# Performance work log

Measured on AMD Instinct MI355X. Metric: run time of the kernel, lower is better.

Reference implementation:

```python
import jax, jax.numpy as jnp
import numpy as np

B, NUM_RX, NUM_CHIRPS, SAMPLES = 16, 4, 64, 256
D_BINS, R_BINS = 64, 256


def _conv3d(x, w, b, pad):
    y = jax.lax.conv_general_dilated(x, w, (1, 1, 1), pad,
                                     dimension_numbers=('NCDHW', 'OIDHW', 'NCDHW'))
    return y + b[None, :, None, None, None]


def _conv2d(x, w, b, pad):
    y = jax.lax.conv_general_dilated(x, w, (1, 1), pad,
                                     dimension_numbers=('NCHW', 'OIHW', 'NCHW'))
    return y + b[None, :, None, None]


def _bn2(x, s, t):
    return x * s[None, :, None, None] + t[None, :, None, None]


def _bn3(x, s, t):
    return x * s[None, :, None, None, None] + t[None, :, None, None, None]


def _upsample_bilinear_ac(x, oh, ow):
    # torch Upsample(mode='bilinear', align_corners=True)
    _, _, h, w = x.shape
    ph = jnp.linspace(0.0, h - 1.0, oh)
    pw = jnp.linspace(0.0, w - 1.0, ow)
    h0 = jnp.clip(jnp.floor(ph).astype(jnp.int32), 0, h - 1)
    h1 = jnp.clip(h0 + 1, 0, h - 1)
    fh = ph - h0
    w0 = jnp.clip(jnp.floor(pw).astype(jnp.int32), 0, w - 1)
    w1 = jnp.clip(w0 + 1, 0, w - 1)
    fw = pw - w0
    x = x[:, :, h0, :] * (1.0 - fh)[None, None, :, None] + x[:, :, h1, :] * fh[None, None, :, None]
    x = x[:, :, :, w0] * (1.0 - fw) + x[:, :, :, w1] * fw
    return x


def setup_inputs() -> dict:
    ks = iter(jax.random.split(jax.random.key(0), 80))

    def nrm(shape, s=0.05):
        return s * jax.random.normal(next(ks), shape, dtype=jnp.float32)

    inp = {'x': jax.random.normal(next(ks), (B, NUM_RX, NUM_CHIRPS, SAMPLES, 2), dtype=jnp.float32)}

    def conv(name, shape):
        inp[name + '_w'] = nrm(shape)
        inp[name + '_b'] = nrm((shape[0],))

    def bn(name, n):  # BatchNorm in inference form folded to scale/shift
        inp[name + '_s'] = 1.0 + nrm((n,), 0.1)
        inp[name + '_t'] = nrm((n,), 0.1)

    conv('tc1', (16, 2, 1, 1, 3)); bn('tc1', 16)
    conv('tc2', (32, 16, 1, 1, 3)); bn('tc2', 32)
    conv('rx', (32, 32, NUM_RX, 1, 1)); bn('rx', 32)
    conv('cc1', (64, 32 * NUM_CHIRPS, 3, 3)); bn('cc1', 64)
    conv('cc2', (64, 64, 3, 3)); bn('cc2', 64)
    conv('rd1', (128, 64, 3, 3)); bn('rd1', 128)
    conv('rd2', (128, 128, 3, 3)); bn('rd2', 128)
    conv('up1', (64, 128, 3, 3)); bn('up1', 64)
    conv('up2', (32, 64, 3, 3)); bn('up2', 32)
    conv('up3', (1, 32, 1, 1))
    inp['wr'] = jax.random.normal(next(ks), (SAMPLES, R_BINS, 2), dtype=jnp.float32)
    inp['wd'] = jax.random.normal(next(ks), (NUM_CHIRPS, D_BINS, 2), dtype=jnp.float32)
    return inp


def reference(x, tc1_w, tc1_b, tc1_s, tc1_t, tc2_w, tc2_b, tc2_s, tc2_t,
              rx_w, rx_b, rx_s, rx_t, cc1_w, cc1_b, cc1_s, cc1_t,
              cc2_w, cc2_b, cc2_s, cc2_t, rd1_w, rd1_b, rd1_s, rd1_t,
              rd2_w, rd2_b, rd2_s, rd2_t, up1_w, up1_b, up1_s, up1_t,
              up2_w, up2_b, up2_s, up2_t, up3_w, up3_b, wr, wd):
    r = jax.nn.relu
    p3 = [(0, 0), (0, 0), (1, 1)]
    p2 = [(1, 1), (1, 1)]
    h = jnp.transpose(x, (0, 4, 1, 2, 3))                      # [B,2,RX,C,S]
    h = r(_bn3(_conv3d(h, tc1_w, tc1_b, p3), tc1_s, tc1_t))
    h = r(_bn3(_conv3d(h, tc2_w, tc2_b, p3), tc2_s, tc2_t))
    h = r(_bn3(_conv3d(h, rx_w, rx_b, [(0, 0)] * 3), rx_s, rx_t))[:, :, 0]  # [B,32,C,S]
    h = h.reshape(h.shape[0], -1, SAMPLES)[:, :, None, :]      # [B,32*C,1,S]
    h = r(_bn2(_conv2d(h, cc1_w, cc1_b, p2), cc1_s, cc1_t))
    h = r(_bn2(_conv2d(h, cc2_w, cc2_b, p2), cc2_s, cc2_t))
    h = r(_bn2(_conv2d(h, rd1_w, rd1_b, p2), rd1_s, rd1_t))
    h = r(_bn2(_conv2d(h, rd2_w, rd2_b, p2), rd2_s, rd2_t))
    h = _upsample_bilinear_ac(h, D_BINS, R_BINS)               # [B,128,D,R]
    h = r(_bn2(_conv2d(h, up1_w, up1_b, p2), up1_s, up1_t))
    h = r(_bn2(_conv2d(h, up2_w, up2_b, p2), up2_s, up2_t))
    h = jax.nn.sigmoid(_conv2d(h, up3_w, up3_b, [(0, 0), (0, 0)]))  # [B,1,D,R]
    # learnable_fft (input is real: x_imag = 0), loops -> two batched matmuls
    xr = h[:, 0]                                               # [B,D,R]
    rr = jnp.einsum('bcs,sr->bcr', xr, wr[:, :, 0])            # range DFT, real
    ri = jnp.einsum('bcs,sr->bcr', xr, wr[:, :, 1])            # range DFT, imag
    rdr = jnp.einsum('bcr,cd->bdr', rr, wd[:, :, 0]) - jnp.einsum('bcr,cd->bdr', ri, wd[:, :, 1])
    rdi = jnp.einsum('bcr,cd->bdr', rr, wd[:, :, 1]) + jnp.einsum('bcr,cd->bdr', ri, wd[:, :, 0])
    mag = jnp.sqrt(rdr * rdr + rdi * rdi) / (NUM_CHIRPS * SAMPLES)
    out = jnp.clip(h + 0.1 * mag[:, None], 0.0, 1.0)
    return jnp.transpose(out, (0, 2, 3, 1))                    # [B,D,R,1]
```

## Files before the change

kernel.cpp:

```cpp
#include <hip/hip_runtime.h>
#include <math.h>

#define OFF_A      0u
#define OFF_P      8388608u
#define OFF_WCC1   10485760u
#define OFF_BCC1   11010048u
#define OFF_WCC2   11010112u
#define OFF_BCC2   11026496u
#define OFF_WRD1   11026560u
#define OFF_BRD1   11059328u
#define OFF_WRD2   11059456u
#define OFF_BRD2   11124992u
#define OFF_WUP1   11125120u
#define OFF_BUP1   11223424u
#define OFF_WUP2   11223488u
#define OFF_BUP2   11346368u
#define OFF_WRX    11346400u
#define OFF_W1F    11350496u
#define OFF_B1F    11350592u
#define OFF_W2F    11350608u
#define OFF_B2F    11352144u
#define OFF_BRXF   11352176u
#define OFF_R      0u
#define OFF_H      524288u

__device__ __forceinline__ void fma4(float4& a, const float4& x, float w) {
  a.x = fmaf(x.x, w, a.x); a.y = fmaf(x.y, w, a.y);
  a.z = fmaf(x.z, w, a.z); a.w = fmaf(x.w, w, a.w);
}

__global__ __launch_bounds__(256) void k_repack_front(
    const float* __restrict__ tc1_w, const float* __restrict__ tc1_b, const float* __restrict__ tc1_s, const float* __restrict__ tc1_t,
    const float* __restrict__ tc2_w, const float* __restrict__ tc2_b, const float* __restrict__ tc2_s, const float* __restrict__ tc2_t,
    const float* __restrict__ rx_w, const float* __restrict__ rx_b, const float* __restrict__ rx_s, const float* __restrict__ rx_t,
    float* __restrict__ ws)
{
  const int tid = blockIdx.x * blockDim.x + threadIdx.x;
  const int nth = gridDim.x * blockDim.x;
  for (int i = tid; i < 96; i += nth) ws[OFF_W1F + i] = tc1_w[i] * tc1_s[i/6];
  for (int i = tid; i < 16; i += nth) ws[OFF_B1F + i] = tc1_b[i]*tc1_s[i] + tc1_t[i];
  for (int i = tid; i < 1536; i += nth) {
    int oc = i & 31, r = i >> 5, k = r % 3, ic = r / 3;
    ws[OFF_W2F + i] = tc2_w[oc*48 + ic*3 + k] * tc2_s[oc];
  }
  for (int i = tid; i < 32; i += nth) ws[OFF_B2F + i] = tc2_b[i]*tc2_s[i] + tc2_t[i];
  for (int i = tid; i < 4096; i += nth) {
    int oc = i & 31, ic = (i >> 5) & 31, rxi = i >> 10;
    ws[OFF_WRX + i] = rx_w[(oc*32 + ic)*4 + rxi] * rx_s[oc];
  }
  for (int i = tid; i < 32; i += nth) ws[OFF_BRXF + i] = rx_b[i]*rx_s[i] + rx_t[i];
}

__global__ __launch_bounds__(256, 4) void k_front(
    const float* __restrict__ x, const float* __restrict__ ws_c, float* __restrict__ ws,
    const float* __restrict__ cc1_w, const float* __restrict__ cc1_b, const float* __restrict__ cc1_s, const float* __restrict__ cc1_t,
    const float* __restrict__ cc2_w, const float* __restrict__ cc2_b, const float* __restrict__ cc2_s, const float* __restrict__ cc2_t,
    const float* __restrict__ rd1_w, const float* __restrict__ rd1_b, const float* __restrict__ rd1_s, const float* __restrict__ rd1_t,
    const float* __restrict__ rd2_w, const float* __restrict__ rd2_b, const float* __restrict__ rd2_s, const float* __restrict__ rd2_t,
    const float* __restrict__ up1_w, const float* __restrict__ up1_b, const float* __restrict__ up1_s, const float* __restrict__ up1_t,
    const float* __restrict__ up2_w, const float* __restrict__ up2_b, const float* __restrict__ up2_s, const float* __restrict__ up2_t,
    float* __restrict__ A)
{
  __shared__ float t1s[16][258];
  const int tid = threadIdx.x;

  if (blockIdx.x < 64) {
    const int t = blockIdx.x * 256 + tid;
    const int nth = 64 * 256;
    for (int i = t; i < 2048*64*4; i += nth) {
      int k = i & 3, oc = (i >> 2) & 63, c2 = i >> 8;
      ws[OFF_WCC1 + i] = (k < 3) ? cc1_w[((oc*2048 + c2)*3 + 1)*3 + k] * cc1_s[oc] : 0.f;
    }
    for (int i = t; i < 64; i += nth) ws[OFF_BCC1 + i] = cc1_b[i]*cc1_s[i] + cc1_t[i];
    for (int i = t; i < 64*64; i += nth) {
      int oc = i & 63, ic = i >> 6;
      float4 v;
      v.x = cc2_w[(oc*64 + ic)*9 + 3] * cc2_s[oc];
      v.y = cc2_w[(oc*64 + ic)*9 + 4] * cc2_s[oc];
      v.z = cc2_w[(oc*64 + ic)*9 + 5] * cc2_s[oc];
      v.w = 0.f;
      ((float4*)(ws + OFF_WCC2))[i] = v;
    }
    for (int i = t; i < 64; i += nth) ws[OFF_BCC2 + i] = cc2_b[i]*cc2_s[i] + cc2_t[i];
    for (int i = t; i < 64*128; i += nth) {
      int oc = i & 127, ic = i >> 7;
      float4 v;
      v.x = rd1_w[(oc*64 + ic)*9 + 3] * rd1_s[oc];
      v.y = rd1_w[(oc*64 + ic)*9 + 4] * rd1_s[oc];
      v.z = rd1_w[(oc*64 + ic)*9 + 5] * rd1_s[oc];
      v.w = 0.f;
      ((float4*)(ws + OFF_WRD1))[i] = v;
    }
    for (int i = t; i < 128; i += nth) ws[OFF_BRD1 + i] = rd1_b[i]*rd1_s[i] + rd1_t[i];
    for (int i = t; i < 128*128; i += nth) {
      int oc = i & 127, ic = i >> 7;
      float4 v;
      v.x = rd2_w[(oc*128 + ic)*9 + 3] * rd2_s[oc];
      v.y = rd2_w[(oc*128 + ic)*9 + 4] * rd2_s[oc];
      v.z = rd2_w[(oc*128 + ic)*9 + 5] * rd2_s[oc];
      v.w = 0.f;
      ((float4*)(ws + OFF_WRD2))[i] = v;
    }
    for (int i = t; i < 128; i += nth) ws[OFF_BRD2 + i] = rd2_b[i]*rd2_s[i] + rd2_t[i];
    for (int i = t; i < 3*128*64; i += nth) {
      int oc = i & 63, ic = (i >> 6) & 127, v = i >> 13;
      const int m = (v == 0) ? 6 : (v == 1) ? 7 : 3;
      float4 o = make_float4(0.f, 0.f, 0.f, 0.f);
      for (int kh = 0; kh < 3; ++kh)
        if ((m >> kh) & 1) {
          o.x += up1_w[((oc*128 + ic)*3 + kh)*3 + 0];
          o.y += up1_w[((oc*128 + ic)*3 + kh)*3 + 1];
          o.z += up1_w[((oc*128 + ic)*3 + kh)*3 + 2];
        }
      o.x *= up1_s[oc]; o.y *= up1_s[oc]; o.z *= up1_s[oc];
      ((float4*)(ws + OFF_WUP1))[i] = o;
    }
    for (int i = t; i < 64; i += nth) ws[OFF_BUP1 + i] = up1_b[i]*up1_s[i] + up1_t[i];
    for (int i = t; i < 5*3*64*32; i += nth) {
      int oc = i & 31, ic = (i >> 5) & 63, tt = i >> 11;
      int src = tt % 3, v = tt / 3;
      const int MASKS[15] = {2,4,0,  1,6,0,  0,7,0,  0,3,4,  0,1,2};
      const int m = MASKS[v*3 + src];
      float4 o = make_float4(0.f, 0.f, 0.f, 0.f);
      for (int kh = 0; kh < 3; ++kh)
        if ((m >> kh) & 1) {
          o.x += up2_w[((oc*64 + ic)*3 + kh)*3 + 0];
          o.y += up2_w[((oc*64 + ic)*3 + kh)*3 + 1];
          o.z += up2_w[((oc*64 + ic)*3 + kh)*3 + 2];
        }
      o.x *= up2_s[oc]; o.y *= up2_s[oc]; o.z *= up2_s[oc];
      ((float4*)(ws + OFF_WUP2))[i] = o;
    }
    for (int i = t; i < 32; i += nth) ws[OFF_BUP2 + i] = up2_b[i]*up2_s[i] + up2_t[i];
    return;
  }

  const int bb = blockIdx.x - 64;
  const int b = bb >> 6, chirp = bb & 63;
  const int s = tid;

  if (tid < 32) { int o = tid & 15; int c = (tid >> 4) ? 257 : 0; t1s[o][c] = 0.f; }

  const float* w1f  = ws_c + OFF_W1F;
  const float* b1f  = ws_c + OFF_B1F;
  const float* w2f  = ws_c + OFF_W2F;
  const float* b2f  = ws_c + OFF_B2F;
  const float* wrxf = ws_c + OFF_WRX;
  const float* brxf = ws_c + OFF_BRXF;

  float acc[32];
  #pragma unroll
  for (int j = 0; j < 32; ++j) acc[j] = 0.f;

  #pragma unroll 1
  for (int rxi = 0; rxi < 4; ++rxi) {
    {
      const float2* xb2 = (const float2*)(x + ((size_t)(((b*4 + rxi)*64 + chirp)*256) << 1));
      float2 xm = xb2[s];
      float2 xl = xb2[(s == 0) ? 0 : (s - 1)];
      float2 xr = xb2[(s == 255) ? 255 : (s + 1)];
      if (s == 0)   { xl.x = 0.f; xl.y = 0.f; }
      if (s == 255) { xr.x = 0.f; xr.y = 0.f; }
      #pragma unroll 4
      for (int o = 0; o < 16; ++o) {
        const float* w = w1f + o*6;
        float v = b1f[o];
        v = fmaf(xl.x, w[0], v);
        v = fmaf(xm.x, w[1], v);
        v = fmaf(xr.x, w[2], v);
        v = fmaf(xl.y, w[3], v);
        v = fmaf(xm.y, w[4], v);
        v = fmaf(xr.y, w[5], v);
        t1s[o][s+1] = fmaxf(v, 0.f);
      }
    }
    __syncthreads();

    float t2[32];
    #pragma unroll
    for (int j = 0; j < 32; ++j) t2[j] = b2f[j];
    #pragma unroll 2
    for (int ic = 0; ic < 16; ++ic) {
      float tl = t1s[ic][s];
      float tm = t1s[ic][s+1];
      float tr = t1s[ic][s+2];
      const float* w = w2f + ic*96;
      #pragma unroll
      for (int oc = 0; oc < 32; ++oc)
        t2[oc] = fmaf(tl, w[oc], fmaf(tm, w[32+oc], fmaf(tr, w[64+oc], t2[oc])));
    }
    #pragma unroll
    for (int j = 0; j < 32; ++j) t2[j] = fmaxf(t2[j], 0.f);

    const float* wr0 = wrxf + rxi*1024;
    #pragma unroll 4
    for (int ic = 0; ic < 32; ++ic) {
      float tv = t2[ic];
      const float* w = wr0 + ic*32;
      #pragma unroll
      for (int oc = 0; oc < 32; ++oc)
        acc[oc] = fmaf(tv, w[oc], acc[oc]);
    }
    __syncthreads();
  }

  #pragma unroll 4
  for (int oc = 0; oc < 32; ++oc) {
    float v = fmaxf(acc[oc] + brxf[oc], 0.f);
    A[(size_t)((b*2048 + oc*64 + chirp)*256) + s] = v;
  }
}

__global__ __launch_bounds__(256) void k_cc1(
    const float* __restrict__ A, const float* __restrict__ wp, float* __restrict__ P)
{
  __shared__ __align__(16) float As[256][36];
  const int tid = threadIdx.x;
  const int ks = blockIdx.x & 7;
  const int stile = (blockIdx.x >> 3) & 7;
  const int b = blockIdx.x >> 6;
  const int s0 = stile * 32;
  const int oc = tid & 63;
  const int sg = tid >> 6;
  const int cbase = ks * 256;
  const float4* w4 = (const float4*)wp;

  for (int i = tid; i < 256*36; i += 256) {
    int c = i / 36, si = i - c*36;
    int sA = s0 - 1 + si;
    float v = 0.f;
    if (si < 34 && sA >= 0 && sA < 256)
      v = A[(size_t)(b*2048 + cbase + c)*256 + sA];
    As[c][si] = v;
  }
  __syncthreads();

  const int sb = sg * 8;
  float4 acc0 = make_float4(0.f,0.f,0.f,0.f);
  float4 acc1 = make_float4(0.f,0.f,0.f,0.f);
  #pragma unroll 4
  for (int c = 0; c < 256; ++c) {
    float4 w = w4[(size_t)(cbase + c)*64 + oc];
    float4 a0 = *(const float4*)&As[c][sb];
    float4 a1 = *(const float4*)&As[c][sb + 4];
    float2 a2 = *(const float2*)&As[c][sb + 8];
    acc0.x = fmaf(a0.x,w.x, fmaf(a0.y,w.y, fmaf(a0.z,w.z, acc0.x)));
    acc0.y = fmaf(a0.y,w.x, fmaf(a0.z,w.y, fmaf(a0.w,w.z, acc0.y)));
    acc0.z = fmaf(a0.z,w.x, fmaf(a0.w,w.y, fmaf(a1.x,w.z, acc0.z)));
    acc0.w = fmaf(a0.w,w.x, fmaf(a1.x,w.y, fmaf(a1.y,w.z, acc0.w)));
    acc1.x = fmaf(a1.x,w.x, fmaf(a1.y,w.y, fmaf(a1.z,w.z, acc1.x)));
    acc1.y = fmaf(a1.y,w.x, fmaf(a1.z,w.y, fmaf(a1.w,w.z, acc1.y)));
    acc1.z = fmaf(a1.z,w.x, fmaf(a1.w,w.y, fmaf(a2.x,w.z, acc1.z)));
    acc1.w = fmaf(a1.w,w.x, fmaf(a2.x,w.y, fmaf(a2.y,w.z, acc1.w)));
  }
  float* Pk = P + ((size_t)(ks*16 + b)*256)*64;
  int s = s0 + sb;
  Pk[(size_t)(s+0)*64 + oc] = acc0.x;
  Pk[(size_t)(s+1)*64 + oc] = acc0.y;
  Pk[(size_t)(s+2)*64 + oc] = acc0.z;
  Pk[(size_t)(s+3)*64 + oc] = acc0.w;
  Pk[(size_t)(s+4)*64 + oc] = acc1.x;
  Pk[(size_t)(s+5)*64 + oc] = acc1.y;
  Pk[(size_t)(s+6)*64 + oc] = acc1.z;
  Pk[(size_t)(s+7)*64 + oc] = acc1.w;
}

__global__ __launch_bounds__(256) void k_mid(
    const float* __restrict__ P, const float* __restrict__ bcc1,
    const float* __restrict__ wcc2, const float* __restrict__ bcc2,
    const float* __restrict__ wrd1, const float* __restrict__ brd1,
    const float* __restrict__ wrd2, const float* __restrict__ brd2,
    float* __restrict__ R)
{
  __shared__ __align__(16) float c1s[64][20];
  __shared__ __align__(16) float c2s[64][20];
  __shared__ __align__(16) float r1s[128][12];
  const int tid = threadIdx.x;
  const int b = blockIdx.x >> 5;
  const int s0 = (blockIdx.x & 31) * 8;
  const float4* wc2 = (const float4*)wcc2;
  const float4* wr1 = (const float4*)wrd1;
  const float4* wr2 = (const float4*)wrd2;

  for (int i = tid; i < 64*14; i += 256) {
    int ic = i & 63, si = i >> 6;
    int sA = s0 - 3 + si;
    float v = 0.f;
    if (sA >= 0 && sA < 256) {
      float a = bcc1[ic];
      #pragma unroll
      for (int ksp = 0; ksp < 8; ++ksp)
        a += P[((size_t)(ksp*16 + b)*256 + sA)*64 + ic];
      v = fmaxf(a, 0.f);
    }
    c1s[ic][si] = v;
  }
  __syncthreads();

  {
    const int g = tid >> 6, oc = tid & 63;
    if (g < 3) {
      float bb = bcc2[oc];
      float4 acc = make_float4(bb, bb, bb, bb);
      #pragma unroll 4
      for (int ic = 0; ic < 64; ++ic) {
        float4 w = wc2[ic*64 + oc];
        float4 ca = *(const float4*)&c1s[ic][g*4];
        float2 cb = *(const float2*)&c1s[ic][g*4 + 4];
        acc.x = fmaf(ca.x,w.x, fmaf(ca.y,w.y, fmaf(ca.z,w.z, acc.x)));
        acc.y = fmaf(ca.y,w.x, fmaf(ca.z,w.y, fmaf(ca.w,w.z, acc.y)));
        acc.z = fmaf(ca.z,w.x, fmaf(ca.w,w.y, fmaf(cb.x,w.z, acc.z)));
        acc.w = fmaf(ca.w,w.x, fmaf(cb.x,w.y, fmaf(cb.y,w.z, acc.w)));
      }
      c2s[oc][g*4+0] = fmaxf(acc.x, 0.f);
      c2s[oc][g*4+1] = fmaxf(acc.y, 0.f);
      c2s[oc][g*4+2] = fmaxf(acc.z, 0.f);
      c2s[oc][g*4+3] = fmaxf(acc.w, 0.f);
    } else {
      int oc2 = tid - 192;
      c2s[oc2][12] = 0.f;
      c2s[oc2][13] = 0.f;
    }
  }
  __syncthreads();

  for (int it = tid; it < 384; it += 256) {
    const int oc = it & 127, g = it >> 7;
    float bb = brd1[oc];
    float4 acc = make_float4(bb, bb, bb, bb);
    #pragma unroll 4
    for (int ic = 0; ic < 64; ++ic) {
      float4 w = wr1[ic*128 + oc];
      float4 ca = *(const float4*)&c2s[ic][g*4];
      float2 cb = *(const float2*)&c2s[ic][g*4 + 4];
      acc.x = fmaf(ca.x,w.x, fmaf(ca.y,w.y, fmaf(ca.z,w.z, acc.x)));
      acc.y = fmaf(ca.y,w.x, fmaf(ca.z,w.y, fmaf(ca.w,w.z, acc.y)));
      acc.z = fmaf(ca.z,w.x, fmaf(ca.w,w.y, fmaf(cb.x,w.z, acc.z)));
      acc.w = fmaf(ca.w,w.x, fmaf(cb.x,w.y, fmaf(cb.y,w.z, acc.w)));
    }
    if (g*4 + 0 < 12) r1s[oc][g*4+0] = fmaxf(acc.x, 0.f);
    if (g*4 + 1 < 12) r1s[oc][g*4+1] = fmaxf(acc.y, 0.f);
    if (g*4 + 2 < 12) r1s[oc][g*4+2] = fmaxf(acc.z, 0.f);
    if (g*4 + 3 < 12) r1s[oc][g*4+3] = fmaxf(acc.w, 0.f);
  }
  __syncthreads();

  {
    const int g = tid >> 7, oc = tid & 127;
    float bb = brd2[oc];
    float4 acc = make_float4(bb, bb, bb, bb);
    #pragma unroll 4
    for (int ic = 0; ic < 128; ++ic) {
      float4 w = wr2[ic*128 + oc];
      float4 ca = *(const float4*)&r1s[ic][g*4];
      float2 cb = *(const float2*)&r1s[ic][g*4 + 4];
      acc.x = fmaf(ca.x,w.x, fmaf(ca.y,w.y, fmaf(ca.z,w.z, acc.x)));
      acc.y = fmaf(ca.y,w.x, fmaf(ca.z,w.y, fmaf(ca.w,w.z, acc.y)));
      acc.z = fmaf(ca.z,w.x, fmaf(ca.w,w.y, fmaf(cb.x,w.z, acc.z)));
      acc.w = fmaf(ca.w,w.x, fmaf(cb.x,w.y, fmaf(cb.y,w.z, acc.w)));
    }
    int s = s0 + g*4;
    R[((size_t)b*256 + s+0)*128 + oc] = fmaxf(acc.x, 0.f);
    R[((size_t)b*256 + s+1)*128 + oc] = fmaxf(acc.y, 0.f);
    R[((size_t)b*256 + s+2)*128 + oc] = fmaxf(acc.z, 0.f);
    R[((size_t)b*256 + s+3)*128 + oc] = fmaxf(acc.w, 0.f);
  }
}

__global__ __launch_bounds__(192) void k_up(
    const float* __restrict__ R,
    const float* __restrict__ wup1, const float* __restrict__ bup1,
    const float* __restrict__ wup2, const float* __restrict__ bup2,
    const float* __restrict__ up3_w, const float* __restrict__ up3_b,
    float* __restrict__ H)
{
  __shared__ __align__(16) float Rs[128][12];
  __shared__ __align__(16) float u1s[3][64][12];
  __shared__ float u2s[5][32][9];
  const int tid = threadIdx.x;
  const int b = blockIdx.x >> 5;
  const int s0 = (blockIdx.x & 31) * 8;

  for (int i = tid; i < 128*12; i += 192) {
    int ic = i & 127, si = i >> 7;
    int sA = s0 - 2 + si;
    Rs[ic][si] = (sA >= 0 && sA < 256) ? R[((size_t)b*256 + sA)*128 + ic] : 0.f;
  }
  __syncthreads();

  {
    const int vi = tid >> 6, oc = tid & 63;
    const float4* w4 = (const float4*)wup1;
    float a[10];
    float bb = bup1[oc];
    #pragma unroll
    for (int p = 0; p < 10; ++p) a[p] = bb;
    #pragma unroll 4
    for (int ic = 0; ic < 128; ++ic) {
      float4 w = w4[(vi*128 + ic)*64 + oc];
      float4 ra = *(const float4*)&Rs[ic][0];
      float4 rb = *(const float4*)&Rs[ic][4];
      float4 rc = *(const float4*)&Rs[ic][8];
      float r[12] = {ra.x,ra.y,ra.z,ra.w, rb.x,rb.y,rb.z,rb.w, rc.x,rc.y,rc.z,rc.w};
      #pragma unroll
      for (int p = 0; p < 10; ++p)
        a[p] = fmaf(r[p],w.x, fmaf(r[p+1],w.y, fmaf(r[p+2],w.z, a[p])));
    }
    #pragma unroll
    for (int p = 0; p < 10; ++p) u1s[vi][oc][p] = fmaxf(a[p], 0.f);
    u1s[vi][oc][10] = 0.f; u1s[vi][oc][11] = 0.f;
  }
  __syncthreads();

  if (tid < 160) {
    const int v = tid >> 5, oc = tid & 31;
    const float4* w4 = (const float4*)wup2;
    float a[8];
    float bb = bup2[oc];
    #pragma unroll
    for (int p = 0; p < 8; ++p) a[p] = bb;
    for (int src = 0; src < 3; ++src) {
      #pragma unroll 4
      for (int ic = 0; ic < 64; ++ic) {
        float4 w = w4[((v*3 + src)*64 + ic)*32 + oc];
        float4 ua = *(const float4*)&u1s[src][ic][0];
        float4 ub = *(const float4*)&u1s[src][ic][4];
        float2 uc = *(const float2*)&u1s[src][ic][8];
        float r[10] = {ua.x,ua.y,ua.z,ua.w, ub.x,ub.y,ub.z,ub.w, uc.x,uc.y};
        #pragma unroll
        for (int p = 0; p < 8; ++p)
          a[p] = fmaf(r[p],w.x, fmaf(r[p+1],w.y, fmaf(r[p+2],w.z, a[p])));
      }
    }
    #pragma unroll
    for (int p = 0; p < 8; ++p) u2s[v][oc][p] = fmaxf(a[p], 0.f);
  }
  __syncthreads();

  if (tid < 40) {
    int v = tid >> 3, j = tid & 7;
    float a = up3_b[0];
    for (int ic = 0; ic < 32; ++ic)
      a = fmaf(u2s[v][ic][j], up3_w[ic], a);
    H[(size_t)(b*5 + v)*256 + s0 + j] = 1.f / (1.f + expf(-a));
  }
}

__global__ __launch_bounds__(256) void k_spec(
    const float* __restrict__ H, const float* __restrict__ wr, const float* __restrict__ wd,
    float* __restrict__ out)
{
  __shared__ float hs[5][256];
  __shared__ float S0[64], S1[64];
  __shared__ float wds[4][64][2];
  __shared__ float ps[16][16][10];
  __shared__ float rred[16][10];
  const int tid = threadIdx.x;
  const int b = blockIdx.x >> 4;
  const int rt = blockIdx.x & 15;
  const int r0 = rt * 16;

  for (int i = tid; i < 1280; i += 256) hs[i >> 8][i & 255] = H[(size_t)b*1280 + i];
  if (tid < 64) {
    const float2* wd2 = (const float2*)wd;
    float a0 = 0.f, a1 = 0.f;
    for (int c = 2; c <= 61; ++c) {
      float2 v = wd2[c*64 + tid];
      a0 += v.x; a1 += v.y;
    }
    S0[tid] = a0; S1[tid] = a1;
  }
  for (int i = tid; i < 512; i += 256) {
    int row = i >> 7, rem = i & 127, d = rem >> 1, comp = rem & 1;
    int c = (row < 2) ? row : (60 + row);
    wds[row][d][comp] = wd[(c*64 + d)*2 + comp];
  }
  __syncthreads();

  {
    const int rl = tid & 15;
    const int sq = tid >> 4;
    const int r = r0 + rl;
    float rr[5] = {0,0,0,0,0}, ri[5] = {0,0,0,0,0};
    const float2* wr2p = (const float2*)wr;
    for (int s = sq*16; s < sq*16 + 16; ++s) {
      float2 w = wr2p[s*256 + r];
      #pragma unroll
      for (int k = 0; k < 5; ++k) {
        float hv = hs[k][s];
        rr[k] = fmaf(hv, w.x, rr[k]);
        ri[k] = fmaf(hv, w.y, ri[k]);
      }
    }
    #pragma unroll
    for (int k = 0; k < 5; ++k) {
      ps[sq][rl][k]     = rr[k];
      ps[sq][rl][5 + k] = ri[k];
    }
  }
  __syncthreads();

  if (tid < 160) {
    const int rl = tid & 15, k = tid >> 4;
    float a = 0.f;
    #pragma unroll
    for (int sq = 0; sq < 16; ++sq) a += ps[sq][rl][k];
    rred[rl][k] = a;
  }
  __syncthreads();

  {
    const int rl = tid & 15, dg = tid >> 4;
    const int r = r0 + rl;
    float Rr[5], Ri[5];
    #pragma unroll
    for (int k = 0; k < 5; ++k) { Rr[k] = rred[rl][k]; Ri[k] = rred[rl][5 + k]; }
    for (int dd = 0; dd < 4; ++dd) {
      int d = dg*4 + dd;
      float w0r = wds[0][d][0], w0i = wds[0][d][1];
      float w1r = wds[1][d][0], w1i = wds[1][d][1];
      float w2r = wds[2][d][0], w2i = wds[2][d][1];
      float w3r = wds[3][d][0], w3i = wds[3][d][1];
      float s0v = S0[d], s1v = S1[d];
      float rdr = Rr[0]*w0r + Rr[1]*w1r + Rr[2]*s0v + Rr[3]*w2r + Rr[4]*w3r
                - Ri[0]*w0i - Ri[1]*w1i - Ri[2]*s1v - Ri[3]*w2i - Ri[4]*w3i;
      float rdi = Rr[0]*w0i + Rr[1]*w1i + Rr[2]*s1v + Rr[3]*w2i + Rr[4]*w3i
                + Ri[0]*w0r + Ri[1]*w1r + Ri[2]*s0v + Ri[3]*w2r + Ri[4]*w3r;
      float mag = sqrtf(rdr*rdr + rdi*rdi) * (1.0f / 16384.0f);
      int v = (d == 0) ? 0 : (d == 1) ? 1 : (d <= 61) ? 2 : ((d == 62) ? 3 : 4);
      float o = hs[v][r] + 0.1f * mag;
      out[(size_t)b*16384 + d*256 + r] = fminf(fmaxf(o, 0.f), 1.f);
    }
  }
}

extern "C" void kernel_launch(void* const* d_in, const int* in_sizes, int n_in,
                              void* d_out, int out_size, void* d_ws, size_t ws_size,
                              hipStream_t stream)
{
  const float* x     = (const float*)d_in[0];
  const float* tc1_w = (const float*)d_in[1];  const float* tc1_b = (const float*)d_in[2];
  const float* tc1_s = (const float*)d_in[3];  const float* tc1_t = (const float*)d_in[4];
  const float* tc2_w = (const float*)d_in[5];  const float* tc2_b = (const float*)d_in[6];
  const float* tc2_s = (const float*)d_in[7];  const float* tc2_t = (const float*)d_in[8];
  const float* rx_w  = (const float*)d_in[9];  const float* rx_b  = (const float*)d_in[10];
  const float* rx_s  = (const float*)d_in[11]; const float* rx_t  = (const float*)d_in[12];
  const float* cc1_w = (const float*)d_in[13]; const float* cc1_b = (const float*)d_in[14];
  const float* cc1_s = (const float*)d_in[15]; const float* cc1_t = (const float*)d_in[16];
  const float* cc2_w = (const float*)d_in[17]; const float* cc2_b = (const float*)d_in[18];
  const float* cc2_s = (const float*)d_in[19]; const float* cc2_t = (const float*)d_in[20];
  const float* rd1_w = (const float*)d_in[21]; const float* rd1_b = (const float*)d_in[22];
  const float* rd1_s = (const float*)d_in[23]; const float* rd1_t = (const float*)d_in[24];
  const float* rd2_w = (const float*)d_in[25]; const float* rd2_b = (const float*)d_in[26];
  const float* rd2_s = (const float*)d_in[27]; const float* rd2_t = (const float*)d_in[28];
  const float* up1_w = (const float*)d_in[29]; const float* up1_b = (const float*)d_in[30];
  const float* up1_s = (const float*)d_in[31]; const float* up1_t = (const float*)d_in[32];
  const float* up2_w = (const float*)d_in[33]; const float* up2_b = (const float*)d_in[34];
  const float* up2_s = (const float*)d_in[35]; const float* up2_t = (const float*)d_in[36];
  const float* up3_w = (const float*)d_in[37]; const float* up3_b = (const float*)d_in[38];
  const float* wr    = (const float*)d_in[39];
  const float* wd    = (const float*)d_in[40];
  float* ws  = (float*)d_ws;
  float* out = (float*)d_out;

  k_repack_front<<<8, 256, 0, stream>>>(tc1_w, tc1_b, tc1_s, tc1_t,
                                        tc2_w, tc2_b, tc2_s, tc2_t,
                                        rx_w, rx_b, rx_s, rx_t, ws);
  k_front<<<1088, 256, 0, stream>>>(x, ws, ws,
                                    cc1_w, cc1_b, cc1_s, cc1_t,
                                    cc2_w, cc2_b, cc2_s, cc2_t,
                                    rd1_w, rd1_b, rd1_s, rd1_t,
                                    rd2_w, rd2_b, rd2_s, rd2_t,
                                    up1_w, up1_b, up1_s, up1_t,
                                    up2_w, up2_b, up2_s, up2_t,
                                    ws + OFF_A);
  k_cc1<<<1024, 256, 0, stream>>>(ws + OFF_A, ws + OFF_WCC1, ws + OFF_P);
  k_mid<<<512, 256, 0, stream>>>(ws + OFF_P, ws + OFF_BCC1,
                                 ws + OFF_WCC2, ws + OFF_BCC2,
                                 ws + OFF_WRD1, ws + OFF_BRD1,
                                 ws + OFF_WRD2, ws + OFF_BRD2, ws + OFF_R);
  k_up<<<512, 192, 0, stream>>>(ws + OFF_R, ws + OFF_WUP1, ws + OFF_BUP1,
                                ws + OFF_WUP2, ws + OFF_BUP2, up3_w, up3_b, ws + OFF_H);
  k_spec<<<256, 256, 0, stream>>>(ws + OFF_H, wr, wd, out);
}
```

Baseline: 339.1 us.

## Fuse mid and upsample kernels with halo recompute; double-buffer front t1s per RX pair

New measurement: 357.6 us. 5.5% more time.

```diff
diff --git a/kernel.cpp b/kernel.cpp
--- a/kernel.cpp
+++ b/kernel.cpp
@@ -21,8 +21,7 @@
 #define OFF_W2F    11350608u
 #define OFF_B2F    11352144u
 #define OFF_BRXF   11352176u
-#define OFF_R      0u
-#define OFF_H      524288u
+#define OFF_H      0u
 
 __device__ __forceinline__ void fma4(float4& a, const float4& x, float w) {
   a.x = fmaf(x.x, w, a.x); a.y = fmaf(x.y, w, a.y);
@@ -61,7 +60,7 @@
     const float* __restrict__ up2_w, const float* __restrict__ up2_b, const float* __restrict__ up2_s, const float* __restrict__ up2_t,
     float* __restrict__ A)
 {
-  __shared__ float t1s[16][258];
+  __shared__ float t1s[2][16][258];
   const int tid = threadIdx.x;
 
   if (blockIdx.x < 64) {
@@ -139,7 +138,11 @@
   const int b = bb >> 6, chirp = bb & 63;
   const int s = tid;
 
-  if (tid < 32) { int o = tid & 15; int c = (tid >> 4) ? 257 : 0; t1s[o][c] = 0.f; }
+  if (tid < 64) {
+    int o = tid & 15, rr = (tid >> 4) & 1;
+    int c = (tid >> 5) ? 257 : 0;
+    t1s[rr][o][c] = 0.f;
+  }
 
   const float* w1f  = ws_c + OFF_W1F;
   const float* b1f  = ws_c + OFF_B1F;
@@ -153,8 +156,10 @@
   for (int j = 0; j < 32; ++j) acc[j] = 0.f;
 
   #pragma unroll 1
-  for (int rxi = 0; rxi < 4; ++rxi) {
-    {
+  for (int r2 = 0; r2 < 2; ++r2) {
+    #pragma unroll
+    for (int rr = 0; rr < 2; ++rr) {
+      const int rxi = r2*2 + rr;
       const float2* xb2 = (const float2*)(x + ((size_t)(((b*4 + rxi)*64 + chirp)*256) << 1));
       float2 xm = xb2[s];
       float2 xl = xb2[(s == 0) ? 0 : (s - 1)];
@@ -171,35 +176,39 @@
         v = fmaf(xl.y, w[3], v);
         v = fmaf(xm.y, w[4], v);
         v = fmaf(xr.y, w[5], v);
-        t1s[o][s+1] = fmaxf(v, 0.f);
+        t1s[rr][o][s+1] = fmaxf(v, 0.f);
       }
     }
     __syncthreads();
 
-    float t2[32];
-    #pragma unroll
-    for (int j = 0; j < 32; ++j) t2[j] = b2f[j];
-    #pragma unroll 2
-    for (int ic = 0; ic < 16; ++ic) {
-      float tl = t1s[ic][s];
-      float tm = t1s[ic][s+1];
-      float tr = t1s[ic][s+2];
-      const float* w = w2f + ic*96;
-      #pragma unroll
-      for (int oc = 0; oc < 32; ++oc)
-        t2[oc] = fmaf(tl, w[oc], fmaf(tm, w[32+oc], fmaf(tr, w[64+oc], t2[oc])));
-    }
-    #pragma unroll
-    for (int j = 0; j < 32; ++j) t2[j] = fmaxf(t2[j], 0.f);
-
-    const float* wr0 = wrxf + rxi*1024;
-    #pragma unroll 4
-    for (int ic = 0; ic < 32; ++ic) {
-      float tv = t2[ic];
-      const float* w = wr0 + ic*32;
-      #pragma unroll
-      for (int oc = 0; oc < 32; ++oc)
-        acc[oc] = fmaf(tv, w[oc], acc[oc]);
+    #pragma unroll 1
+    for (int rr = 0; rr < 2; ++rr) {
+      const int rxi = r2*2 + rr;
+      float t2[32];
+      #pragma unroll
+      for (int j = 0; j < 32; ++j) t2[j] = b2f[j];
+      #pragma unroll 2
+      for (int ic = 0; ic < 16; ++ic) {
+        float tl = t1s[rr][ic][s];
+        float tm = t1s[rr][ic][s+1];
+        float tr = t1s[rr][ic][s+2];
+        const float* w = w2f + ic*96;
+        #pragma unroll
+        for (int oc = 0; oc < 32; ++oc)
+          t2[oc] = fmaf(tl, w[oc], fmaf(tm, w[32+oc], fmaf(tr, w[64+oc], t2[oc])));
+      }
+      #pragma unroll
+      for (int j = 0; j < 32; ++j) t2[j] = fmaxf(t2[j], 0.f);
+
+      const float* wr0 = wrxf + rxi*1024;
+      #pragma unroll 4
+      for (int ic = 0; ic < 32; ++ic) {
+        float tv = t2[ic];
+        const float* w = wr0 + ic*32;
+        #pragma unroll
+        for (int oc = 0; oc < 32; ++oc)
+          acc[oc] = fmaf(tv, w[oc], acc[oc]);
+      }
     }
     __syncthreads();
   }
@@ -265,26 +274,37 @@
   Pk[(size_t)(s+7)*64 + oc] = acc1.w;
 }
 
-__global__ __launch_bounds__(256) void k_mid(
+__global__ __launch_bounds__(256) void k_midup(
     const float* __restrict__ P, const float* __restrict__ bcc1,
     const float* __restrict__ wcc2, const float* __restrict__ bcc2,
     const float* __restrict__ wrd1, const float* __restrict__ brd1,
     const float* __restrict__ wrd2, const float* __restrict__ brd2,
-    float* __restrict__ R)
+    const float* __restrict__ wup1, const float* __restrict__ bup1,
+    const float* __restrict__ wup2, const float* __restrict__ bup2,
+    const float* __restrict__ up3_w, const float* __restrict__ up3_b,
+    float* __restrict__ H)
 {
-  __shared__ __align__(16) float c1s[64][20];
-  __shared__ __align__(16) float c2s[64][20];
-  __shared__ __align__(16) float r1s[128][12];
+  __shared__ __align__(16) float bufA[2560];
+  __shared__ __align__(16) float bufB[2560];
+  __shared__ float u2s[5][32][9];
+  float* c1s = bufA;
+  float* c2s = bufA + 1280;
+  float* r1s = bufB;
+  float* Rls = bufA;
+  float* u1s = bufB;
+
   const int tid = threadIdx.x;
   const int b = blockIdx.x >> 5;
   const int s0 = (blockIdx.x & 31) * 8;
   const float4* wc2 = (const float4*)wcc2;
   const float4* wr1 = (const float4*)wrd1;
   const float4* wr2 = (const float4*)wrd2;
-
-  for (int i = tid; i < 64*14; i += 256) {
+  const float4* wu1 = (const float4*)wup1;
+  const float4* wu2 = (const float4*)wup2;
+
+  for (int i = tid; i < 18*64; i += 256) {
     int ic = i & 63, si = i >> 6;
-    int sA = s0 - 3 + si;
+    int sA = s0 - 5 + si;
     float v = 0.f;
     if (sA >= 0 && sA < 256) {
       float a = bcc1[ic];
@@ -293,128 +313,127 @@
         a += P[((size_t)(ksp*16 + b)*256 + sA)*64 + ic];
       v = fmaxf(a, 0.f);
     }
-    c1s[ic][si] = v;
+    c1s[ic*20 + si] = v;
   }
   __syncthreads();
 
   {
     const int g = tid >> 6, oc = tid & 63;
-    if (g < 3) {
-      float bb = bcc2[oc];
-      float4 acc = make_float4(bb, bb, bb, bb);
-      #pragma unroll 4
-      for (int ic = 0; ic < 64; ++ic) {
-        float4 w = wc2[ic*64 + oc];
-        float4 ca = *(const float4*)&c1s[ic][g*4];
-        float2 cb = *(const float2*)&c1s[ic][g*4 + 4];
-        acc.x = fmaf(ca.x,w.x, fmaf(ca.y,w.y, fmaf(ca.z,w.z, acc.x)));
-        acc.y = fmaf(ca.y,w.x, fmaf(ca.z,w.y, fmaf(ca.w,w.z, acc.y)));
-        acc.z = fmaf(ca.z,w.x, fmaf(ca.w,w.y, fmaf(cb.x,w.z, acc.z)));
-        acc.w = fmaf(ca.w,w.x, fmaf(cb.x,w.y, fmaf(cb.y,w.z, acc.w)));
-      }
-      c2s[oc][g*4+0] = fmaxf(acc.x, 0.f);
-      c2s[oc][g*4+1] = fmaxf(acc.y, 0.f);
-      c2s[oc][g*4+2] = fmaxf(acc.z, 0.f);
-      c2s[oc][g*4+3] = fmaxf(acc.w, 0.f);
-    } else {
-      int oc2 = tid - 192;
-      c2s[oc2][12] = 0.f;
-      c2s[oc2][13] = 0.f;
-    }
-  }
-  __syncthreads();
-
-  for (int it = tid; it < 384; it += 256) {
-    const int oc = it & 127, g = it >> 7;
-    float bb = brd1[oc];
+    float bb = bcc2[oc];
     float4 acc = make_float4(bb, bb, bb, bb);
     #pragma unroll 4
     for (int ic = 0; ic < 64; ++ic) {
-      float4 w = wr1[ic*128 + oc];
-      float4 ca = *(const float4*)&c2s[ic][g*4];
-      float2 cb = *(const float2*)&c2s[ic][g*4 + 4];
+      float4 w = wc2[ic*64 + oc];
+      float4 ca = *(const float4*)&c1s[ic*20 + g*4];
+      float2 cb = *(const float2*)&c1s[ic*20 + g*4 + 4];
       acc.x = fmaf(ca.x,w.x, fmaf(ca.y,w.y, fmaf(ca.z,w.z, acc.x)));
       acc.y = fmaf(ca.y,w.x, fmaf(ca.z,w.y, fmaf(ca.w,w.z, acc.y)));
       acc.z = fmaf(ca.z,w.x, fmaf(ca.w,w.y, fmaf(cb.x,w.z, acc.z)));
       acc.w = fmaf(ca.w,w.x, fmaf(cb.x,w.y, fmaf(cb.y,w.z, acc.w)));
     }
-    if (g*4 + 0 < 12) r1s[oc][g*4+0] = fmaxf(acc.x, 0.f);
-    if (g*4 + 1 < 12) r1s[oc][g*4+1] = fmaxf(acc.y, 0.f);
-    if (g*4 + 2 < 12) r1s[oc][g*4+2] = fmaxf(acc.z, 0.f);
-    if (g*4 + 3 < 12) r1s[oc][g*4+3] = fmaxf(acc.w, 0.f);
+    float r[4] = {acc.x, acc.y, acc.z, acc.w};
+    #pragma unroll
+    for (int j = 0; j < 4; ++j) {
+      int si = g*4 + j, sA = s0 - 4 + si;
+      c2s[oc*20 + si] = (sA >= 0 && sA < 256) ? fmaxf(r[j], 0.f) : 0.f;
+    }
+    c2s[oc*20 + 16 + g] = 0.f;
   }
   __syncthreads();
 
   {
-    const int g = tid >> 7, oc = tid & 127;
+    const int oc = tid & 127, g = tid >> 7;
+    float bb = brd1[oc];
+    float a[8];
+    #pragma unroll
+    for (int j = 0; j < 8; ++j) a[j] = bb;
+    #pragma unroll 4
+    for (int ic = 0; ic < 64; ++ic) {
+      float4 w = wr1[ic*128 + oc];
+      float4 ca = *(const float4*)&c2s[ic*20 + g*8];
+      float4 cb = *(const float4*)&c2s[ic*20 + g*8 + 4];
+      float2 cc = *(const float2*)&c2s[ic*20 + g*8 + 8];
+      float r[10] = {ca.x,ca.y,ca.z,ca.w, cb.x,cb.y,cb.z,cb.w, cc.x,cc.y};
+      #pragma unroll
+      for (int j = 0; j < 8; ++j)
+        a[j] = fmaf(r[j],w.x, fmaf(r[j+1],w.y, fmaf(r[j+2],w.z, a[j])));
+    }
+    #pragma unroll
+    for (int j = 0; j < 8; ++j) {
+      int si = g*8 + j, sA = s0 - 3 + si;
+      if (si < 14)
+        r1s[oc*20 + si] = (sA >= 0 && sA < 256) ? fmaxf(a[j], 0.f) : 0.f;
+    }
+  }
+  #pragma unroll
+  for (int k = 0; k < 3; ++k) {
+    int idx = k*256 + tid;
+    int ic = idx & 127, si = 14 + (idx >> 7);
+    r1s[ic*20 + si] = 0.f;
+  }
+  __syncthreads();
+
+  {
+    const int oc = tid & 127, g = tid >> 7;
     float bb = brd2[oc];
-    float4 acc = make_float4(bb, bb, bb, bb);
+    float a[8];
+    #pragma unroll
+    for (int j = 0; j < 8; ++j) a[j] = bb;
     #pragma unroll 4
     for (int ic = 0; ic < 128; ++ic) {
       float4 w = wr2[ic*128 + oc];
-      float4 ca = *(const float4*)&r1s[ic][g*4];
-      float2 cb = *(const float2*)&r1s[ic][g*4 + 4];
-      acc.x = fmaf(ca.x,w.x, fmaf(ca.y,w.y, fmaf(ca.z,w.z, acc.x)));
-      acc.y = fmaf(ca.y,w.x, fmaf(ca.z,w.y, fmaf(ca.w,w.z, acc.y)));
-      acc.z = fmaf(ca.z,w.x, fmaf(ca.w,w.y, fmaf(cb.x,w.z, acc.z)));
-      acc.w = fmaf(ca.w,w.x, fmaf(cb.x,w.y, fmaf(cb.y,w.z, acc.w)));
-    }
-    int s = s0 + g*4;
-    R[((size_t)b*256 + s+0)*128 + oc] = fmaxf(acc.x, 0.f);
-    R[((size_t)b*256 + s+1)*128 + oc] = fmaxf(acc.y, 0.f);
-    R[((size_t)b*256 + s+2)*128 + oc] = fmaxf(acc.z, 0.f);
-    R[((size_t)b*256 + s+3)*128 + oc] = fmaxf(acc.w, 0.f);
-  }
-}
-
-__global__ __launch_bounds__(192) void k_up(
-    const float* __restrict__ R,
-    const float* __restrict__ wup1, const float* __restrict__ bup1,
-    const float* __restrict__ wup2, const float* __restrict__ bup2,
-    const float* __restrict__ up3_w, const float* __restrict__ up3_b,
-    float* __restrict__ H)
-{
-  __shared__ __align__(16) float Rs[128][12];
-  __shared__ __align__(16) float u1s[3][64][12];
-  __shared__ float u2s[5][32][9];
-  const int tid = threadIdx.x;
-  const int b = blockIdx.x >> 5;
-  const int s0 = (blockIdx.x & 31) * 8;
-
-  for (int i = tid; i < 128*12; i += 192) {
-    int ic = i & 127, si = i >> 7;
-    int sA = s0 - 2 + si;
-    Rs[ic][si] = (sA >= 0 && sA < 256) ? R[((size_t)b*256 + sA)*128 + ic] : 0.f;
+      float4 ca = *(const float4*)&r1s[ic*20 + g*8];
+      float4 cb = *(const float4*)&r1s[ic*20 + g*8 + 4];
+      float2 cc = *(const float2*)&r1s[ic*20 + g*8 + 8];
+      float r[10] = {ca.x,ca.y,ca.z,ca.w, cb.x,cb.y,cb.z,cb.w, cc.x,cc.y};
+      #pragma unroll
+      for (int j = 0; j < 8; ++j)
+        a[j] = fmaf(r[j],w.x, fmaf(r[j+1],w.y, fmaf(r[j+2],w.z, a[j])));
+    }
+    __syncthreads();
+    #pragma unroll
+    for (int j = 0; j < 8; ++j) {
+      int si = g*8 + j, sA = s0 - 2 + si;
+      if (si < 12)
+        Rls[oc*12 + si] = (sA >= 0 && sA < 256) ? fmaxf(a[j], 0.f) : 0.f;
+    }
   }
   __syncthreads();
 
   {
+    float a[10];
     const int vi = tid >> 6, oc = tid & 63;
-    const float4* w4 = (const float4*)wup1;
-    float a[10];
-    float bb = bup1[oc];
-    #pragma unroll
-    for (int p = 0; p < 10; ++p) a[p] = bb;
-    #pragma unroll 4
-    for (int ic = 0; ic < 128; ++ic) {
-      float4 w = w4[(vi*128 + ic)*64 + oc];
-      float4 ra = *(const float4*)&Rs[ic][0];
-      float4 rb = *(const float4*)&Rs[ic][4];
-      float4 rc = *(const float4*)&Rs[ic][8];
-      float r[12] = {ra.x,ra.y,ra.z,ra.w, rb.x,rb.y,rb.z,rb.w, rc.x,rc.y,rc.z,rc.w};
-      #pragma unroll
-      for (int p = 0; p < 10; ++p)
-        a[p] = fmaf(r[p],w.x, fmaf(r[p+1],w.y, fmaf(r[p+2],w.z, a[p])));
-    }
-    #pragma unroll
-    for (int p = 0; p < 10; ++p) u1s[vi][oc][p] = fmaxf(a[p], 0.f);
-    u1s[vi][oc][10] = 0.f; u1s[vi][oc][11] = 0.f;
+    if (vi < 3) {
+      float bb = bup1[oc];
+      #pragma unroll
+      for (int p = 0; p < 10; ++p) a[p] = bb;
+      #pragma unroll 4
+      for (int ic = 0; ic < 128; ++ic) {
+        float4 w = wu1[(vi*128 + ic)*64 + oc];
+        float4 ra = *(const float4*)&Rls[ic*12 + 0];
+        float4 rb = *(const float4*)&Rls[ic*12 + 4];
+        float4 rc = *(const float4*)&Rls[ic*12 + 8];
+        float r[12] = {ra.x,ra.y,ra.z,ra.w, rb.x,rb.y,rb.z,rb.w, rc.x,rc.y,rc.z,rc.w};
+        #pragma unroll
+        for (int p = 0; p < 10; ++p)
+          a[p] = fmaf(r[p],w.x, fmaf(r[p+1],w.y, fmaf(r[p+2],w.z, a[p])));
+      }
+    }
+    __syncthreads();
+    if (vi < 3) {
+      #pragma unroll
+      for (int p = 0; p < 10; ++p) {
+        int sA = s0 - 1 + p;
+        u1s[(vi*64 + oc)*12 + p] = (sA >= 0 && sA < 256) ? fmaxf(a[p], 0.f) : 0.f;
+      }
+      u1s[(vi*64 + oc)*12 + 10] = 0.f;
+      u1s[(vi*64 + oc)*12 + 11] = 0.f;
+    }
   }
   __syncthreads();
 
   if (tid < 160) {
     const int v = tid >> 5, oc = tid & 31;
-    const float4* w4 = (const float4*)wup2;
     float a[8];
     float bb = bup2[oc];
     #pragma unroll
@@ -422,10 +441,10 @@
     for (int src = 0; src < 3; ++src) {
       #pragma unroll 4
       for (int ic = 0; ic < 64; ++ic) {
-        float4 w = w4[((v*3 + src)*64 + ic)*32 + oc];
-        float4 ua = *(const float4*)&u1s[src][ic][0];
-        float4 ub = *(const float4*)&u1s[src][ic][4];
-        float2 uc = *(const float2*)&u1s[src][ic][8];
+        float4 w = wu2[((v*3 + src)*64 + ic)*32 + oc];
+        float4 ua = *(const float4*)&u1s[(src*64 + ic)*12 + 0];
+        float4 ub = *(const float4*)&u1s[(src*64 + ic)*12 + 4];
+        float2 uc = *(const float2*)&u1s[(src*64 + ic)*12 + 8];
         float r[10] = {ua.x,ua.y,ua.z,ua.w, ub.x,ub.y,ub.z,ub.w, uc.x,uc.y};
         #pragma unroll
         for (int p = 0; p < 8; ++p)
@@ -575,11 +594,12 @@
                                     up2_w, up2_b, up2_s, up2_t,
                                     ws + OFF_A);
   k_cc1<<<1024, 256, 0, stream>>>(ws + OFF_A, ws + OFF_WCC1, ws + OFF_P);
-  k_mid<<<512, 256, 0, stream>>>(ws + OFF_P, ws + OFF_BCC1,
-                                 ws + OFF_WCC2, ws + OFF_BCC2,
-                                 ws + OFF_WRD1, ws + OFF_BRD1,
-                                 ws + OFF_WRD2, ws + OFF_BRD2, ws + OFF_R);
-  k_up<<<512, 192, 0, stream>>>(ws + OFF_R, ws + OFF_WUP1, ws + OFF_BUP1,
-                                ws + OFF_WUP2, ws + OFF_BUP2, up3_w, up3_b, ws + OFF_H);
+  k_midup<<<512, 256, 0, stream>>>(ws + OFF_P, ws + OFF_BCC1,
+                                   ws + OFF_WCC2, ws + OFF_BCC2,
+                                   ws + OFF_WRD1, ws + OFF_BRD1,
+                                   ws + OFF_WRD2, ws + OFF_BRD2,
+                                   ws + OFF_WUP1, ws + OFF_BUP1,
+                                   ws + OFF_WUP2, ws + OFF_BUP2,
+                                   up3_w, up3_b, ws + OFF_H);
   k_spec<<<256, 256, 0, stream>>>(ws + OFF_H, wr, wd, out);
 }
```

## Split k_mid across two blocks by rd1 channel half with partial-sum outputs

Applied to the files above, without the earlier changes.

Result: no change. 338.5 us (-0.2%).

```diff
diff --git a/kernel.cpp b/kernel.cpp
--- a/kernel.cpp
+++ b/kernel.cpp
@@ -21,8 +21,9 @@
 #define OFF_W2F    11350608u
 #define OFF_B2F    11352144u
 #define OFF_BRXF   11352176u
-#define OFF_R      0u
-#define OFF_H      524288u
+#define OFF_RP0    0u
+#define OFF_RP1    524288u
+#define OFF_H      1048576u
 
 __device__ __forceinline__ void fma4(float4& a, const float4& x, float w) {
   a.x = fmaf(x.x, w, a.x); a.y = fmaf(x.y, w, a.y);
@@ -270,19 +271,21 @@
     const float* __restrict__ wcc2, const float* __restrict__ bcc2,
     const float* __restrict__ wrd1, const float* __restrict__ brd1,
     const float* __restrict__ wrd2, const float* __restrict__ brd2,
-    float* __restrict__ R)
+    float* __restrict__ Rp0, float* __restrict__ Rp1)
 {
   __shared__ __align__(16) float c1s[64][20];
   __shared__ __align__(16) float c2s[64][20];
-  __shared__ __align__(16) float r1s[128][12];
+  __shared__ __align__(16) float r1s[64][12];
   const int tid = threadIdx.x;
-  const int b = blockIdx.x >> 5;
-  const int s0 = (blockIdx.x & 31) * 8;
+  const int half = blockIdx.x & 1;
+  const int stile = (blockIdx.x >> 1) & 31;
+  const int b = blockIdx.x >> 6;
+  const int s0 = stile * 8;
   const float4* wc2 = (const float4*)wcc2;
   const float4* wr1 = (const float4*)wrd1;
   const float4* wr2 = (const float4*)wrd2;
 
-  for (int i = tid; i < 64*14; i += 256) {
+  for (int i = tid; i < 14*64; i += 256) {
     int ic = i & 63, si = i >> 6;
     int sA = s0 - 3 + si;
     float v = 0.f;
@@ -312,10 +315,12 @@
         acc.z = fmaf(ca.z,w.x, fmaf(ca.w,w.y, fmaf(cb.x,w.z, acc.z)));
         acc.w = fmaf(ca.w,w.x, fmaf(cb.x,w.y, fmaf(cb.y,w.z, acc.w)));
       }
-      c2s[oc][g*4+0] = fmaxf(acc.x, 0.f);
-      c2s[oc][g*4+1] = fmaxf(acc.y, 0.f);
-      c2s[oc][g*4+2] = fmaxf(acc.z, 0.f);
-      c2s[oc][g*4+3] = fmaxf(acc.w, 0.f);
+      float r[4] = {acc.x, acc.y, acc.z, acc.w};
+      #pragma unroll
+      for (int j = 0; j < 4; ++j) {
+        int si = g*4 + j, sA = s0 - 2 + si;
+        c2s[oc][si] = (sA >= 0 && sA < 256) ? fmaxf(r[j], 0.f) : 0.f;
+      }
     } else {
       int oc2 = tid - 192;
       c2s[oc2][12] = 0.f;
@@ -324,34 +329,44 @@
   }
   __syncthreads();
 
-  for (int it = tid; it < 384; it += 256) {
-    const int oc = it & 127, g = it >> 7;
-    float bb = brd1[oc];
+  {
+    const int g = tid >> 6, ocl = tid & 63;
+    if (g < 3) {
+      const int ocg = half*64 + ocl;
+      float bb = brd1[ocg];
+      float4 acc = make_float4(bb, bb, bb, bb);
+      #pragma unroll 4
+      for (int ic = 0; ic < 64; ++ic) {
+        float4 w = wr1[ic*128 + ocg];
+        float4 ca = *(const float4*)&c2s[ic][g*4];
+        float2 cb = *(const float2*)&c2s[ic][g*4 + 4];
+        acc.x = fmaf(ca.x,w.x, fmaf(ca.y,w.y, fmaf(ca.z,w.z, acc.x)));
+        acc.y = fmaf(ca.y,w.x, fmaf(ca.z,w.y, fmaf(ca.w,w.z, acc.y)));
+        acc.z = fmaf(ca.z,w.x, fmaf(ca.w,w.y, fmaf(cb.x,w.z, acc.z)));
+        acc.w = fmaf(ca.w,w.x, fmaf(cb.x,w.y, fmaf(cb.y,w.z, acc.w)));
+      }
+      float r[4] = {acc.x, acc.y, acc.z, acc.w};
+      #pragma unroll
+      for (int j = 0; j < 4; ++j) {
+        int si = g*4 + j, sA = s0 - 1 + si;
+        if (si < 10)
+          r1s[ocl][si] = (sA >= 0 && sA < 256) ? fmaxf(r[j], 0.f) : 0.f;
+      }
+    } else {
+      int oc2 = tid - 192;
+      r1s[oc2][10] = 0.f;
+      r1s[oc2][11] = 0.f;
+    }
+  }
+  __syncthreads();
+
+  {
+    const int g = tid >> 7, oc = tid & 127;
+    float bb = half ? 0.f : brd2[oc];
     float4 acc = make_float4(bb, bb, bb, bb);
     #pragma unroll 4
     for (int ic = 0; ic < 64; ++ic) {
-      float4 w = wr1[ic*128 + oc];
-      float4 ca = *(const float4*)&c2s[ic][g*4];
-      float2 cb = *(const float2*)&c2s[ic][g*4 + 4];
-      acc.x = fmaf(ca.x,w.x, fmaf(ca.y,w.y, fmaf(ca.z,w.z, acc.x)));
-      acc.y = fmaf(ca.y,w.x, fmaf(ca.z,w.y, fmaf(ca.w,w.z, acc.y)));
-      acc.z = fmaf(ca.z,w.x, fmaf(ca.w,w.y, fmaf(cb.x,w.z, acc.z)));
-      acc.w = fmaf(ca.w,w.x, fmaf(cb.x,w.y, fmaf(cb.y,w.z, acc.w)));
-    }
-    if (g*4 + 0 < 12) r1s[oc][g*4+0] = fmaxf(acc.x, 0.f);
-    if (g*4 + 1 < 12) r1s[oc][g*4+1] = fmaxf(acc.y, 0.f);
-    if (g*4 + 2 < 12) r1s[oc][g*4+2] = fmaxf(acc.z, 0.f);
-    if (g*4 + 3 < 12) r1s[oc][g*4+3] = fmaxf(acc.w, 0.f);
-  }
-  __syncthreads();
-
-  {
-    const int g = tid >> 7, oc = tid & 127;
-    float bb = brd2[oc];
-    float4 acc = make_float4(bb, bb, bb, bb);
-    #pragma unroll 4
-    for (int ic = 0; ic < 128; ++ic) {
-      float4 w = wr2[ic*128 + oc];
+      float4 w = wr2[(half*64 + ic)*128 + oc];
       float4 ca = *(const float4*)&r1s[ic][g*4];
       float2 cb = *(const float2*)&r1s[ic][g*4 + 4];
       acc.x = fmaf(ca.x,w.x, fmaf(ca.y,w.y, fmaf(ca.z,w.z, acc.x)));
@@ -359,16 +374,17 @@
       acc.z = fmaf(ca.z,w.x, fmaf(ca.w,w.y, fmaf(cb.x,w.z, acc.z)));
       acc.w = fmaf(ca.w,w.x, fmaf(cb.x,w.y, fmaf(cb.y,w.z, acc.w)));
     }
+    float* Rp = half ? Rp1 : Rp0;
     int s = s0 + g*4;
-    R[((size_t)b*256 + s+0)*128 + oc] = fmaxf(acc.x, 0.f);
-    R[((size_t)b*256 + s+1)*128 + oc] = fmaxf(acc.y, 0.f);
-    R[((size_t)b*256 + s+2)*128 + oc] = fmaxf(acc.z, 0.f);
-    R[((size_t)b*256 + s+3)*128 + oc] = fmaxf(acc.w, 0.f);
+    Rp[((size_t)b*256 + s+0)*128 + oc] = acc.x;
+    Rp[((size_t)b*256 + s+1)*128 + oc] = acc.y;
+    Rp[((size_t)b*256 + s+2)*128 + oc] = acc.z;
+    Rp[((size_t)b*256 + s+3)*128 + oc] = acc.w;
   }
 }
 
 __global__ __launch_bounds__(192) void k_up(
-    const float* __restrict__ R,
+    const float* __restrict__ Rp0, const float* __restrict__ Rp1,
     const float* __restrict__ wup1, const float* __restrict__ bup1,
     const float* __restrict__ wup2, const float* __restrict__ bup2,
     const float* __restrict__ up3_w, const float* __restrict__ up3_b,
@@ -384,7 +400,12 @@
   for (int i = tid; i < 128*12; i += 192) {
     int ic = i & 127, si = i >> 7;
     int sA = s0 - 2 + si;
-    Rs[ic][si] = (sA >= 0 && sA < 256) ? R[((size_t)b*256 + sA)*128 + ic] : 0.f;
+    float v = 0.f;
+    if (sA >= 0 && sA < 256) {
+      size_t idx = ((size_t)b*256 + sA)*128 + ic;
+      v = fmaxf(Rp0[idx] + Rp1[idx], 0.f);
+    }
+    Rs[ic][si] = v;
   }
   __syncthreads();
 
@@ -407,7 +428,10 @@
         a[p] = fmaf(r[p],w.x, fmaf(r[p+1],w.y, fmaf(r[p+2],w.z, a[p])));
     }
     #pragma unroll
-    for (int p = 0; p < 10; ++p) u1s[vi][oc][p] = fmaxf(a[p], 0.f);
+    for (int p = 0; p < 10; ++p) {
+      int sA = s0 - 1 + p;
+      u1s[vi][oc][p] = (sA >= 0 && sA < 256) ? fmaxf(a[p], 0.f) : 0.f;
+    }
     u1s[vi][oc][10] = 0.f; u1s[vi][oc][11] = 0.f;
   }
   __syncthreads();
@@ -575,11 +599,14 @@
                                     up2_w, up2_b, up2_s, up2_t,
                                     ws + OFF_A);
   k_cc1<<<1024, 256, 0, stream>>>(ws + OFF_A, ws + OFF_WCC1, ws + OFF_P);
-  k_mid<<<512, 256, 0, stream>>>(ws + OFF_P, ws + OFF_BCC1,
-                                 ws + OFF_WCC2, ws + OFF_BCC2,
-                                 ws + OFF_WRD1, ws + OFF_BRD1,
-                                 ws + OFF_WRD2, ws + OFF_BRD2, ws + OFF_R);
-  k_up<<<512, 192, 0, stream>>>(ws + OFF_R, ws + OFF_WUP1, ws + OFF_BUP1,
-                                ws + OFF_WUP2, ws + OFF_BUP2, up3_w, up3_b, ws + OFF_H);
+  k_mid<<<1024, 256, 0, stream>>>(ws + OFF_P, ws + OFF_BCC1,
+                                  ws + OFF_WCC2, ws + OFF_BCC2,
+                                  ws + OFF_WRD1, ws + OFF_BRD1,
+                                  ws + OFF_WRD2, ws + OFF_BRD2,
+                                  ws + OFF_RP0, ws + OFF_RP1);
+  k_up<<<512, 192, 0, stream>>>(ws + OFF_RP0, ws + OFF_RP1,
+                                ws + OFF_WUP1, ws + OFF_BUP1,
+                                ws + OFF_WUP2, ws + OFF_BUP2,
+                                up3_w, up3_b, ws + OFF_H);
   k_spec<<<256, 256, 0, stream>>>(ws + OFF_H, wr, wd, out);
 }
```
